# Kernel optimization log

Measured on AMD Instinct MI355X. Metric: run time of the kernel, lower is better.

## Reference

```python
import jax, jax.numpy as jnp
import numpy as np

D, H, WIN, OUT = 3, 64, 8, 32
B, T = 128, 129
IU, JU = np.triu_indices(D, k=1)  # Lyndon pairs i<j at depth 2


def setup_inputs() -> dict:
    key = jax.random.key(0)
    ks = jax.random.split(key, 10)
    ts = jnp.broadcast_to(jnp.linspace(0.0, 1.0, T), (B, T))
    # path-like control values: cumulative sum of small increments
    x = jnp.cumsum(0.1 * jax.random.normal(ks[0], (B, T, D)), axis=1)
    def lin(k, o, i):
        return jax.random.normal(k, (o, i), dtype=jnp.float32) * (1.0 / np.sqrt(i))
    return {
        "ts": ts, "x": x,
        "W0": lin(ks[1], 128, D), "b0": jnp.zeros((128,), jnp.float32),
        "W1": lin(ks[2], 128, 128), "b1": jnp.zeros((128,), jnp.float32),
        "W2": lin(ks[3], H, 128), "b2": jnp.zeros((H,), jnp.float32),
        "V0": lin(ks[4], 128, H), "c0": jnp.zeros((128,), jnp.float32),
        "V1": lin(ks[5], 128, 128), "c1": jnp.zeros((128,), jnp.float32),
        "V2": lin(ks[6], D * H, 128), "c2": jnp.zeros((D * H,), jnp.float32),
        "R": lin(ks[7], OUT, H), "rb": jnp.zeros((OUT,), jnp.float32),
    }


def reference(ts, x, W0, b0, W1, b1, W2, b2, V0, c0, V1, c1, V2, c2, R, rb):
    sp = jax.nn.softplus

    def init_mlp(v):  # R^D -> R^H, Euclidean retract = identity
        return W2 @ sp(W1 @ sp(W0 @ v + b0) + b1) + b2

    def vf_flat(y):  # R^H -> R^{D*H}, final tanh (split_multi_vector_field)
        return jnp.tanh(V2 @ sp(V1 @ sp(V0 @ y + c0) + c1) + c2)

    def F(y):
        # level-1 fields f_i(y) as rows of m: (D, H)
        m = vf_flat(y).reshape(D, H)
        # J[a, b] = D f_b(y) . f_a(y)  via JVPs in directions f_a
        J = jax.vmap(lambda v: jax.jvp(vf_flat, (y,), (v,))[1].reshape(D, H))(m)
        # Lyndon level-2 brackets [f_i, f_j] = Df_j.f_i - Df_i.f_j
        br = J[IU, JU] - J[JU, IU]  # (D*(D-1)/2, H)
        return jnp.concatenate([m, br], axis=0).T  # (H, logsig_size)

    def logsigs_fn(xs):  # depth-2 log-signatures over disjoint windows
        nw = (T - 1) // WIN
        idx = (np.arange(nw) * WIN)[:, None] + np.arange(WIN + 1)[None, :]
        win = xs[idx]
        lvl1 = win[:, -1] - win[:, 0]       # increments
        rel = win[:, :-1] - win[:, :1]      # path relative to window start
        dv = win[:, 1:] - win[:, :-1]       # increments within window
        a = jnp.einsum('nki,nkj->nij', rel, dv)
        area = 0.5 * (a - jnp.swapaxes(a, 1, 2))  # Levy areas
        return jnp.concatenate([lvl1, area[:, IU, JU]], axis=1)

    def solve_one(t, xs):
        h0 = init_mlp(xs[0])
        ls = logsigs_fn(xs)                       # (nw, L)
        t_sig = t[::WIN]                          # window knot times
        slopes = ls / (t_sig[1:] - t_sig[:-1])[:, None]  # dz/dt per window
        slope_steps = jnp.repeat(slopes, WIN, axis=0)    # (T-1, L)
        dts = t[1:] - t[:-1]

        def step(y, inp):  # Heun integration of dy = F(y) dz/dt dt
            dt, s = inp
            k1 = F(y) @ s
            k2 = F(y + dt * k1) @ s
            yn = y + 0.5 * dt * (k1 + k2)
            return yn, yn

        _, ys = jax.lax.scan(step, h0, (dts, slope_steps))
        hidden = jnp.concatenate([h0[None], ys], axis=0)  # (T, H)
        return jnp.tanh(hidden @ R.T + rb)                # evolving readout

    return jax.vmap(solve_one)(ts, x)  # (B, T, OUT)
```

## Files before the change

kernel.cpp:

```cpp
#include <hip/hip_runtime.h>
#include <math.h>

#define BB 128
#define TT 129
#define NSTEP 128
#define NW 16
#define WINW 8
#define OUTD 32

typedef _Float16 h2_t __attribute__((ext_vector_type(2)));

__device__ __forceinline__ float fast_rcp(float v){ return __builtin_amdgcn_rcpf(v); }
__device__ __forceinline__ float softplus_f(float v){ return fmaxf(v,0.f)+__logf(1.f+__expf(-fabsf(v))); }
__device__ __forceinline__ float sigmoid_f(float v){ return fast_rcp(1.f+__expf(-v)); }
__device__ __forceinline__ float tanh_f(float v){
    float ax=fminf(fabsf(v),15.f); float e=__expf(2.f*ax);
    float r=1.f-2.f*fast_rcp(e+1.f); return copysignf(r,v);
}
__device__ __forceinline__ float pack2(float a,float b){
    h2_t h; h.x=(_Float16)a; h.y=(_Float16)b; return __builtin_bit_cast(float,h);
}
__device__ __forceinline__ float dot2c(float wc,float ac,float acc){
    return __builtin_amdgcn_fdot2(__builtin_bit_cast(h2_t,wc),__builtin_bit_cast(h2_t,ac),acc,false);
}
__device__ __forceinline__ float dot2q(float4 wq,float4 aq,float acc){
    acc=dot2c(wq.x,aq.x,acc); acc=dot2c(wq.y,aq.y,acc);
    acc=dot2c(wq.z,aq.z,acc); acc=dot2c(wq.w,aq.w,acc); return acc;
}
#define DOT4(acc,Wv,Av) acc += (Wv).x*(Av).x + (Wv).y*(Av).y + (Wv).z*(Av).z + (Wv).w*(Av).w
#define PIN4(q) asm volatile("" : "+v"((q).x), "+v"((q).y), "+v"((q).z), "+v"((q).w))

#define DPPF(x,ctrl) __builtin_bit_cast(float, __builtin_amdgcn_update_dpp(0, __builtin_bit_cast(int,(x)), (ctrl), 0xF, 0xF, true))
__device__ __forceinline__ float dpp_xor1(float x){ return DPPF(x,0xB1); }
__device__ __forceinline__ float dpp_xor2(float x){ return DPPF(x,0x4E); }
__device__ __forceinline__ float dpp_hmir(float x){ return DPPF(x,0x141); }

__global__ __launch_bounds__(256, 1)
void ncde_solve(const float* __restrict__ ts, const float* __restrict__ x,
                const float* __restrict__ W0, const float* __restrict__ b0,
                const float* __restrict__ W1, const float* __restrict__ b1,
                const float* __restrict__ W2, const float* __restrict__ b2,
                const float* __restrict__ V0, const float* __restrict__ c0,
                const float* __restrict__ V1, const float* __restrict__ c1,
                const float* __restrict__ V2, const float* __restrict__ c2,
                const float* __restrict__ R, const float* __restrict__ rb,
                float* __restrict__ out)
{
    const int b = blockIdx.x;
    const int tid = threadIdx.x;
    const int row2 = tid >> 1, half = tid & 1;
    const int row4 = 128 + (tid >> 2), quad = tid & 3;
    const int prow = tid >> 3, poct = tid & 7;

    __shared__ __align__(16) float RSh[OUTD*68];
    __shared__ __align__(16) float ySh[64], k1Sh[64];
    __shared__ __align__(16) float yp[32], y2p[32];
    __shared__ __align__(16) float a0p[64], a1p[64];
    __shared__ __align__(16) float mp[96];
    __shared__ __align__(16) float u0p[3][64], u1p[3][64];
    __shared__ float mSh[192];
    __shared__ float JfSh[3][192];
    __shared__ float slopesSh[NW][6];
    __shared__ float dtsSh[NSTEP];

    float4 v0p4[4];
    float4 v1p4[8];
    float4 v2p4[8];
    float4 v2q4[4];
    {
        const float4* p0 = (const float4*)(V0 + row2*64 + half*32);
        #pragma unroll
        for (int k=0;k<4;k++){
            float4 a=p0[2*k], c=p0[2*k+1];
            float4 r; r.x=pack2(a.x,a.y); r.y=pack2(a.z,a.w); r.z=pack2(c.x,c.y); r.w=pack2(c.z,c.w);
            v0p4[k]=r;
        }
        const float4* p1 = (const float4*)(V1 + row2*128 + half*64);
        #pragma unroll
        for (int k=0;k<8;k++){
            float4 a=p1[2*k], c=p1[2*k+1];
            float4 r; r.x=pack2(a.x,a.y); r.y=pack2(a.z,a.w); r.z=pack2(c.x,c.y); r.w=pack2(c.z,c.w);
            v1p4[k]=r;
        }
        const float4* p2 = (const float4*)(V2 + row2*128 + half*64);
        #pragma unroll
        for (int k=0;k<8;k++){
            float4 a=p2[2*k], c=p2[2*k+1];
            float4 r; r.x=pack2(a.x,a.y); r.y=pack2(a.z,a.w); r.z=pack2(c.x,c.y); r.w=pack2(c.z,c.w);
            v2p4[k]=r;
        }
        #pragma unroll
        for (int j=0;j<4;j++){
            int g=(quad+j)&3;
            const float4* pg = (const float4*)(V2 + row4*128 + quad*32 + g*8);
            float4 a=pg[0], c=pg[1];
            float4 r; r.x=pack2(a.x,a.y); r.y=pack2(a.z,a.w); r.z=pack2(c.x,c.y); r.w=pack2(c.z,c.w);
            v2q4[j]=r;
        }
        #pragma unroll
        for (int k=0;k<4;k++) PIN4(v0p4[k]);
        #pragma unroll
        for (int k=0;k<8;k++) PIN4(v1p4[k]);
        #pragma unroll
        for (int k=0;k<8;k++) PIN4(v2p4[k]);
        #pragma unroll
        for (int k=0;k<4;k++) PIN4(v2q4[k]);
    }
    const float c0r = c0[row2], c1r = c1[row2], c2a = c2[row2], c2b = c2[row4];
    const float rbp = rb[prow];

    for (int i=tid; i<OUTD*64; i+=256) RSh[(i>>6)*68 + (i&63)] = R[i];
    const float* tsb = ts + b*TT;
    for (int i=tid; i<NSTEP; i+=256) dtsSh[i] = tsb[i+1] - tsb[i];

    if (tid < NW) {
        const int w = tid;
        const float* xs = x + (size_t)(b*TT + w*WINW)*3;
        float x0c[3] = {xs[0], xs[1], xs[2]};
        float prev[3] = {x0c[0], x0c[1], x0c[2]};
        float am01=0.f, am02=0.f, am12=0.f, am10=0.f, am20=0.f, am21=0.f;
        #pragma unroll
        for (int k=0;k<WINW;k++) {
            float cur[3] = {xs[(k+1)*3+0], xs[(k+1)*3+1], xs[(k+1)*3+2]};
            float rel[3], dv[3];
            #pragma unroll
            for (int c=0;c<3;c++){ rel[c]=prev[c]-x0c[c]; dv[c]=cur[c]-prev[c]; }
            am01 += rel[0]*dv[1]; am10 += rel[1]*dv[0];
            am02 += rel[0]*dv[2]; am20 += rel[2]*dv[0];
            am12 += rel[1]*dv[2]; am21 += rel[2]*dv[1];
            prev[0]=cur[0]; prev[1]=cur[1]; prev[2]=cur[2];
        }
        const float invden = 1.f/(tsb[(w+1)*WINW] - tsb[w*WINW]);
        slopesSh[w][0] = (prev[0]-x0c[0])*invden;
        slopesSh[w][1] = (prev[1]-x0c[1])*invden;
        slopesSh[w][2] = (prev[2]-x0c[2])*invden;
        slopesSh[w][3] = 0.5f*(am01-am10)*invden;
        slopesSh[w][4] = 0.5f*(am02-am20)*invden;
        slopesSh[w][5] = 0.5f*(am12-am21)*invden;
    }

    if (tid < 128) {
        const float xv0 = x[(size_t)b*TT*3+0];
        const float xv1 = x[(size_t)b*TT*3+1];
        const float xv2 = x[(size_t)b*TT*3+2];
        float acc = b0[tid] + W0[tid*3]*xv0 + W0[tid*3+1]*xv1 + W0[tid*3+2]*xv2;
        mSh[tid] = softplus_f(acc);
    }
    __syncthreads();
    if (tid < 128) {
        float acc = b1[tid];
        const float4* r = (const float4*)(W1 + tid*128);
        #pragma unroll 8
        for (int k=0;k<32;k++){ float4 wv=r[k]; float4 av=*(const float4*)&mSh[4*k]; DOT4(acc,wv,av); }
        JfSh[0][tid] = softplus_f(acc);
    }
    __syncthreads();
    if (tid < 64) {
        float acc = b2[tid];
        const float4* r = (const float4*)(W2 + tid*128);
        #pragma unroll 8
        for (int k=0;k<32;k++){ float4 wv=r[k]; float4 av=*(const float4*)&JfSh[0][4*k]; DOT4(acc,wv,av); }
        ySh[tid] = acc;
        float p = dpp_xor1(acc);
        if (!(tid & 1)) yp[tid>>1] = pack2(acc, p);
    }
    __syncthreads();

    float sig0r=0.f, sig1r=0.f, dtanAr=0.f, dtanBr=0.f;

    const int tlo = (tid < 128) ? 1 : 0;

    auto Feval = [&](const float* ypIn, bool first, float dt, int w) {
        {
            float zA=0.f, zB=0.f;
            const float4* yb = (const float4*)ypIn + half*4;
            zA=dot2q(v0p4[0],yb[0],zA); zB=dot2q(v0p4[1],yb[1],zB);
            zA=dot2q(v0p4[2],yb[2],zA); zB=dot2q(v0p4[3],yb[3],zB);
            float z = zA + zB;
            z += dpp_xor1(z);
            z += c0r;
            float a = softplus_f(z);
            sig0r = sigmoid_f(z);
            if (!half) ((_Float16*)a0p)[row2] = (_Float16)a;
        }
        __syncthreads();
        {
            float zA=0.f, zB=0.f;
            const float4* ab = (const float4*)a0p + half*8;
            #pragma unroll
            for (int k=0;k<4;k++){ zA=dot2q(v1p4[k],ab[k],zA); }
            #pragma unroll
            for (int k=4;k<8;k++){ zB=dot2q(v1p4[k],ab[k],zB); }
            float z = zA + zB;
            z += dpp_xor1(z);
            z += c1r;
            float a = softplus_f(z);
            sig1r = sigmoid_f(z);
            if (!half) ((_Float16*)a1p)[row2] = (_Float16)a;
        }
        __syncthreads();
        {
            float zA=0.f, zB=0.f;
            const float4* ab = (const float4*)a1p + half*8;
            #pragma unroll
            for (int k=0;k<4;k++){ zA=dot2q(v2p4[k],ab[k],zA); }
            #pragma unroll
            for (int k=4;k<8;k++){ zB=dot2q(v2p4[k],ab[k],zB); }
            float z = zA + zB;
            z += dpp_xor1(z);
            z += c2a;
            float mm = tanh_f(z);
            dtanAr = 1.f - mm*mm;
            if (!half){ mSh[row2]=mm; ((_Float16*)mp)[row2]=(_Float16)mm; }

            float zq = 0.f;
            const float4* a4 = (const float4*)a1p;
            #pragma unroll
            for (int j=0;j<4;j++){ zq=dot2q(v2q4[j], a4[quad*4 + ((quad+j)&3)], zq); }
            zq += dpp_xor1(zq);
            zq += dpp_xor2(zq);
            zq += c2b;
            float mq = tanh_f(zq);
            dtanBr = 1.f - mq*mq;
            if (!quad){ mSh[row4]=mq; ((_Float16*)mp)[row4]=(_Float16)mq; }
        }
        __syncthreads();
        {
            float t0=0.f,t1=0.f,t2=0.f;
            const float4* m0 = (const float4*)mp + half*4;
            const float4* m1 = (const float4*)mp + 8  + half*4;
            const float4* m2 = (const float4*)mp + 16 + half*4;
            #pragma unroll
            for (int k=0;k<4;k++){ t0=dot2q(v0p4[k],m0[k],t0); t1=dot2q(v0p4[k],m1[k],t1); t2=dot2q(v0p4[k],m2[k],t2); }
            t0 += dpp_xor1(t0);
            t1 += dpp_xor1(t1);
            t2 += dpp_xor1(t2);
            if (!half){
                ((_Float16*)&u0p[0][0])[row2]=(_Float16)(sig0r*t0);
                ((_Float16*)&u0p[1][0])[row2]=(_Float16)(sig0r*t1);
                ((_Float16*)&u0p[2][0])[row2]=(_Float16)(sig0r*t2);
            }
        }
        __syncthreads();
        {
            float t0=0.f,t1=0.f,t2=0.f;
            const float4* q0 = (const float4*)&u0p[0][0] + half*8;
            const float4* q1 = (const float4*)&u0p[1][0] + half*8;
            const float4* q2 = (const float4*)&u0p[2][0] + half*8;
            #pragma unroll
            for (int k=0;k<8;k++){ t0=dot2q(v1p4[k],q0[k],t0); t1=dot2q(v1p4[k],q1[k],t1); t2=dot2q(v1p4[k],q2[k],t2); }
            t0 += dpp_xor1(t0);
            t1 += dpp_xor1(t1);
            t2 += dpp_xor1(t2);
            if (!half){
                ((_Float16*)&u1p[0][0])[row2]=(_Float16)(sig1r*t0);
                ((_Float16*)&u1p[1][0])[row2]=(_Float16)(sig1r*t1);
                ((_Float16*)&u1p[2][0])[row2]=(_Float16)(sig1r*t2);
            }
        }
        __syncthreads();
        {
            float tl=0.f, t2v=0.f;
            const float4* ql = (const float4*)&u1p[tlo][0] + half*8;
            const float4* q2 = (const float4*)&u1p[2][0]   + half*8;
            #pragma unroll
            for (int k=0;k<8;k++){ tl=dot2q(v2p4[k],ql[k],tl); t2v=dot2q(v2p4[k],q2[k],t2v); }
            tl  += dpp_xor1(tl);
            t2v += dpp_xor1(t2v);
            if (!half){ JfSh[tlo][row2]=dtanAr*tl; JfSh[2][row2]=dtanAr*t2v; }

            float s0=0.f,s1=0.f;
            const float4* w0 = (const float4*)&u1p[0][0];
            const float4* w1 = (const float4*)&u1p[1][0];
            #pragma unroll
            for (int j=0;j<4;j++){
                const int idx = quad*4 + ((quad+j)&3);
                s0=dot2q(v2q4[j],w0[idx],s0); s1=dot2q(v2q4[j],w1[idx],s1);
            }
            s0 += dpp_xor1(s0); s0 += dpp_xor2(s0);
            s1 += dpp_xor1(s1); s1 += dpp_xor2(s1);
            if (!quad){ JfSh[0][row4]=dtanBr*s0; JfSh[1][row4]=dtanBr*s1; }
        }
        __syncthreads();
        if (tid < 64) {
            const int h = tid;
            const float s0=slopesSh[w][0], s1=slopesSh[w][1], s2=slopesSh[w][2],
                        s3=slopesSh[w][3], s4=slopesSh[w][4], s5=slopesSh[w][5];
            float kk = mSh[h]*s0 + mSh[64+h]*s1 + mSh[128+h]*s2;
            kk += s3*(JfSh[0][64+h]  - JfSh[1][h]);
            kk += s4*(JfSh[0][128+h] - JfSh[2][h]);
            kk += s5*(JfSh[1][128+h] - JfSh[2][64+h]);
            if (first){
                k1Sh[h] = kk;
                float y2 = ySh[h] + dt*kk;
                float p = dpp_xor1(y2);
                if (!(h&1)) y2p[h>>1] = pack2(y2, p);
            } else {
                float yn = ySh[h] + 0.5f*dt*(k1Sh[h] + kk);
                ySh[h] = yn;
                float p = dpp_xor1(yn);
                if (!(h&1)) yp[h>>1] = pack2(yn, p);
            }
        }
        __syncthreads();
    };

    auto proj = [&](int stp) {
        const float4* rr = (const float4*)(RSh + prow*68 + poct*8);
        const float4* yy = (const float4*)(ySh + poct*8);
        float pacc = 0.f;
        DOT4(pacc, rr[0], yy[0]); DOT4(pacc, rr[1], yy[1]);
        pacc += dpp_xor1(pacc);
        pacc += dpp_xor2(pacc);
        pacc += dpp_hmir(pacc);
        if (!poct) out[(size_t)(b*TT + stp)*OUTD + prow] = tanh_f(pacc + rbp);
    };

    for (int step=0; step<NSTEP; ++step) {
        proj(step);
        const float dt = dtsSh[step];
        const int w = step >> 3;
        Feval(yp,  true,  dt, w);
        Feval(y2p, false, dt, w);
    }
    proj(NSTEP);
}

extern "C" void kernel_launch(void* const* d_in, const int* in_sizes, int n_in,
                              void* d_out, int out_size, void* d_ws, size_t ws_size,
                              hipStream_t stream) {
    const float* ts = (const float*)d_in[0];
    const float* x  = (const float*)d_in[1];
    const float* W0 = (const float*)d_in[2];
    const float* b0 = (const float*)d_in[3];
    const float* W1 = (const float*)d_in[4];
    const float* b1 = (const float*)d_in[5];
    const float* W2 = (const float*)d_in[6];
    const float* b2 = (const float*)d_in[7];
    const float* V0 = (const float*)d_in[8];
    const float* c0 = (const float*)d_in[9];
    const float* V1 = (const float*)d_in[10];
    const float* c1 = (const float*)d_in[11];
    const float* V2 = (const float*)d_in[12];
    const float* c2 = (const float*)d_in[13];
    const float* R  = (const float*)d_in[14];
    const float* rb = (const float*)d_in[15];
    float* out = (float*)d_out;

    ncde_solve<<<dim3(BB), dim3(256), 0, stream>>>(
        ts, x, W0, b0, W1, b1, W2, b2, V0, c0, V1, c1, V2, c2, R, rb, out);
}
```

Before: 687.1 us.

## Remap work so each thread quad owns rows across all layers, fusing bracket combine

Reorganises the per-step MLP and JVP work so each group of four threads owns hidden row r together with its 64- and 128-offset partners in every layer. Weights are held in registers in this new row-blocked layout, and reductions use two DPP stages. As a result the Lie-bracket combine and Heun update run in registers in the last stage, with y and k1 kept per thread, instead of going through a separate JfSh/mSh stage and barrier. This removes one __syncthreads per F evaluation and some shared-memory traffic. In exchange it uses more registers per thread and adds extra DPP reduction steps.

After: 617.2 us. -10.2%, faster.

```diff
diff --git a/kernel.cpp b/kernel.cpp
--- a/kernel.cpp
+++ b/kernel.cpp
@@ -28,7 +28,7 @@
     acc=dot2c(wq.z,aq.z,acc); acc=dot2c(wq.w,aq.w,acc); return acc;
 }
 #define DOT4(acc,Wv,Av) acc += (Wv).x*(Av).x + (Wv).y*(Av).y + (Wv).z*(Av).z + (Wv).w*(Av).w
-#define PIN4(q) asm volatile("" : "+v"((q).x), "+v"((q).y), "+v"((q).z), "+v"((q).w))
+#define PIN4(v) asm volatile("" : "+v"((v).x), "+v"((v).y), "+v"((v).z), "+v"((v).w))
 
 #define DPPF(x,ctrl) __builtin_bit_cast(float, __builtin_amdgcn_update_dpp(0, __builtin_bit_cast(int,(x)), (ctrl), 0xF, 0xF, true))
 __device__ __forceinline__ float dpp_xor1(float x){ return DPPF(x,0xB1); }
@@ -48,65 +48,59 @@
 {
     const int b = blockIdx.x;
     const int tid = threadIdx.x;
-    const int row2 = tid >> 1, half = tid & 1;
-    const int row4 = 128 + (tid >> 2), quad = tid & 3;
+    const int r = tid >> 2, q = tid & 3;
     const int prow = tid >> 3, poct = tid & 7;
 
     __shared__ __align__(16) float RSh[OUTD*68];
-    __shared__ __align__(16) float ySh[64], k1Sh[64];
+    __shared__ __align__(16) float ySh[64];
     __shared__ __align__(16) float yp[32], y2p[32];
-    __shared__ __align__(16) float a0p[64], a1p[64];
-    __shared__ __align__(16) float mp[96];
-    __shared__ __align__(16) float u0p[3][64], u1p[3][64];
-    __shared__ float mSh[192];
-    __shared__ float JfSh[3][192];
+    __shared__ __align__(16) float a0H[64], a1H[64];
+    __shared__ __align__(16) float mpH[96];
+    __shared__ __align__(16) float u0H[192], u1H[192];
     __shared__ float slopesSh[NW][6];
     __shared__ float dtsSh[NSTEP];
 
-    float4 v0p4[4];
-    float4 v1p4[8];
-    float4 v2p4[8];
-    float4 v2q4[4];
+    float4 v0c[2][2], v1c[2][4], v2c[3][4];
     {
-        const float4* p0 = (const float4*)(V0 + row2*64 + half*32);
-        #pragma unroll
-        for (int k=0;k<4;k++){
-            float4 a=p0[2*k], c=p0[2*k+1];
-            float4 r; r.x=pack2(a.x,a.y); r.y=pack2(a.z,a.w); r.z=pack2(c.x,c.y); r.w=pack2(c.z,c.w);
-            v0p4[k]=r;
-        }
-        const float4* p1 = (const float4*)(V1 + row2*128 + half*64);
-        #pragma unroll
-        for (int k=0;k<8;k++){
-            float4 a=p1[2*k], c=p1[2*k+1];
-            float4 r; r.x=pack2(a.x,a.y); r.y=pack2(a.z,a.w); r.z=pack2(c.x,c.y); r.w=pack2(c.z,c.w);
-            v1p4[k]=r;
-        }
-        const float4* p2 = (const float4*)(V2 + row2*128 + half*64);
-        #pragma unroll
-        for (int k=0;k<8;k++){
-            float4 a=p2[2*k], c=p2[2*k+1];
-            float4 r; r.x=pack2(a.x,a.y); r.y=pack2(a.z,a.w); r.z=pack2(c.x,c.y); r.w=pack2(c.z,c.w);
-            v2p4[k]=r;
-        }
-        #pragma unroll
-        for (int j=0;j<4;j++){
-            int g=(quad+j)&3;
-            const float4* pg = (const float4*)(V2 + row4*128 + quad*32 + g*8);
-            float4 a=pg[0], c=pg[1];
-            float4 r; r.x=pack2(a.x,a.y); r.y=pack2(a.z,a.w); r.z=pack2(c.x,c.y); r.w=pack2(c.z,c.w);
-            v2q4[j]=r;
-        }
-        #pragma unroll
-        for (int k=0;k<4;k++) PIN4(v0p4[k]);
-        #pragma unroll
-        for (int k=0;k<8;k++) PIN4(v1p4[k]);
-        #pragma unroll
-        for (int k=0;k<8;k++) PIN4(v2p4[k]);
-        #pragma unroll
-        for (int k=0;k<4;k++) PIN4(v2q4[k]);
-    }
-    const float c0r = c0[row2], c1r = c1[row2], c2a = c2[row2], c2b = c2[row4];
+        auto pkld = [](const float* src)->float4{
+            const float4* p=(const float4*)src;
+            float4 a=p[0], c=p[1];
+            float4 rr; rr.x=pack2(a.x,a.y); rr.y=pack2(a.z,a.w); rr.z=pack2(c.x,c.y); rr.w=pack2(c.z,c.w);
+            return rr;
+        };
+        #pragma unroll
+        for (int i=0;i<2;i++){
+            const float* base = V0 + (r+64*i)*64 + q*16;
+            v0c[i][0]=pkld(base); v0c[i][1]=pkld(base+8);
+        }
+        #pragma unroll
+        for (int i=0;i<2;i++){
+            const float* base = V1 + (r+64*i)*128 + q*32;
+            #pragma unroll
+            for (int k=0;k<4;k++) v1c[i][k]=pkld(base+8*k);
+        }
+        #pragma unroll
+        for (int i=0;i<3;i++){
+            const float* base = V2 + (r+64*i)*128 + q*32;
+            #pragma unroll
+            for (int k=0;k<4;k++) v2c[i][k]=pkld(base+8*k);
+        }
+        #pragma unroll
+        for (int i=0;i<2;i++){ PIN4(v0c[i][0]); PIN4(v0c[i][1]); }
+        #pragma unroll
+        for (int i=0;i<2;i++){
+            #pragma unroll
+            for (int k=0;k<4;k++) PIN4(v1c[i][k]);
+        }
+        #pragma unroll
+        for (int i=0;i<3;i++){
+            #pragma unroll
+            for (int k=0;k<4;k++) PIN4(v2c[i][k]);
+        }
+    }
+    const float c0A=c0[r], c0B=c0[64+r];
+    const float c1A=c1[r], c1B=c1[64+r];
+    const float c2A=c2[r], c2B=c2[64+r], c2C=c2[128+r];
     const float rbp = rb[prow];
 
     for (int i=tid; i<OUTD*64; i+=256) RSh[(i>>6)*68 + (i&63)] = R[i];
@@ -144,162 +138,167 @@
         const float xv1 = x[(size_t)b*TT*3+1];
         const float xv2 = x[(size_t)b*TT*3+2];
         float acc = b0[tid] + W0[tid*3]*xv0 + W0[tid*3+1]*xv1 + W0[tid*3+2]*xv2;
-        mSh[tid] = softplus_f(acc);
+        u0H[tid] = softplus_f(acc);
     }
     __syncthreads();
     if (tid < 128) {
         float acc = b1[tid];
-        const float4* r = (const float4*)(W1 + tid*128);
+        const float4* rw = (const float4*)(W1 + tid*128);
         #pragma unroll 8
-        for (int k=0;k<32;k++){ float4 wv=r[k]; float4 av=*(const float4*)&mSh[4*k]; DOT4(acc,wv,av); }
-        JfSh[0][tid] = softplus_f(acc);
+        for (int k=0;k<32;k++){ float4 wv=rw[k]; float4 av=*(const float4*)&u0H[4*k]; DOT4(acc,wv,av); }
+        u1H[tid] = softplus_f(acc);
     }
     __syncthreads();
     if (tid < 64) {
         float acc = b2[tid];
-        const float4* r = (const float4*)(W2 + tid*128);
+        const float4* rw = (const float4*)(W2 + tid*128);
         #pragma unroll 8
-        for (int k=0;k<32;k++){ float4 wv=r[k]; float4 av=*(const float4*)&JfSh[0][4*k]; DOT4(acc,wv,av); }
+        for (int k=0;k<32;k++){ float4 wv=rw[k]; float4 av=*(const float4*)&u1H[4*k]; DOT4(acc,wv,av); }
         ySh[tid] = acc;
-        float p = dpp_xor1(acc);
-        if (!(tid & 1)) yp[tid>>1] = pack2(acc, p);
+        ((_Float16*)yp)[tid] = (_Float16)acc;
     }
     __syncthreads();
 
-    float sig0r=0.f, sig1r=0.f, dtanAr=0.f, dtanBr=0.f;
-
-    const int tlo = (tid < 128) ? 1 : 0;
-
-    auto Feval = [&](const float* ypIn, bool first, float dt, int w) {
-        {
+    float yreg = ySh[r];
+    float k1r = 0.f;
+    float S0,S1,S2,S3,S4,S5;
+
+    auto Feval = [&](const float* ypIn, bool first, float dtc) {
+        float sig0A,sig0B,sig1A,sig1B,mA,mB,mC,dtA,dtB,dtC;
+        {
+            const float4* Y = (const float4*)ypIn + q*2;
+            float4 y0=Y[0], y1=Y[1];
             float zA=0.f, zB=0.f;
-            const float4* yb = (const float4*)ypIn + half*4;
-            zA=dot2q(v0p4[0],yb[0],zA); zB=dot2q(v0p4[1],yb[1],zB);
-            zA=dot2q(v0p4[2],yb[2],zA); zB=dot2q(v0p4[3],yb[3],zB);
-            float z = zA + zB;
-            z += dpp_xor1(z);
-            z += c0r;
-            float a = softplus_f(z);
-            sig0r = sigmoid_f(z);
-            if (!half) ((_Float16*)a0p)[row2] = (_Float16)a;
-        }
-        __syncthreads();
-        {
+            zA=dot2q(v0c[0][0],y0,zA); zA=dot2q(v0c[0][1],y1,zA);
+            zB=dot2q(v0c[1][0],y0,zB); zB=dot2q(v0c[1][1],y1,zB);
+            zA += dpp_xor1(zA); zA += dpp_xor2(zA); zA += c0A;
+            zB += dpp_xor1(zB); zB += dpp_xor2(zB); zB += c0B;
+            sig0A=sigmoid_f(zA); sig0B=sigmoid_f(zB);
+            if (!q){
+                ((_Float16*)a0H)[r]    = (_Float16)softplus_f(zA);
+                ((_Float16*)a0H)[64+r] = (_Float16)softplus_f(zB);
+            }
+        }
+        __syncthreads();
+        {
+            const float4* A = (const float4*)a0H + q*4;
+            float4 a0=A[0],a1=A[1],a2=A[2],a3=A[3];
             float zA=0.f, zB=0.f;
-            const float4* ab = (const float4*)a0p + half*8;
-            #pragma unroll
-            for (int k=0;k<4;k++){ zA=dot2q(v1p4[k],ab[k],zA); }
-            #pragma unroll
-            for (int k=4;k<8;k++){ zB=dot2q(v1p4[k],ab[k],zB); }
-            float z = zA + zB;
-            z += dpp_xor1(z);
-            z += c1r;
-            float a = softplus_f(z);
-            sig1r = sigmoid_f(z);
-            if (!half) ((_Float16*)a1p)[row2] = (_Float16)a;
-        }
-        __syncthreads();
-        {
-            float zA=0.f, zB=0.f;
-            const float4* ab = (const float4*)a1p + half*8;
-            #pragma unroll
-            for (int k=0;k<4;k++){ zA=dot2q(v2p4[k],ab[k],zA); }
-            #pragma unroll
-            for (int k=4;k<8;k++){ zB=dot2q(v2p4[k],ab[k],zB); }
-            float z = zA + zB;
-            z += dpp_xor1(z);
-            z += c2a;
-            float mm = tanh_f(z);
-            dtanAr = 1.f - mm*mm;
-            if (!half){ mSh[row2]=mm; ((_Float16*)mp)[row2]=(_Float16)mm; }
-
-            float zq = 0.f;
-            const float4* a4 = (const float4*)a1p;
-            #pragma unroll
-            for (int j=0;j<4;j++){ zq=dot2q(v2q4[j], a4[quad*4 + ((quad+j)&3)], zq); }
-            zq += dpp_xor1(zq);
-            zq += dpp_xor2(zq);
-            zq += c2b;
-            float mq = tanh_f(zq);
-            dtanBr = 1.f - mq*mq;
-            if (!quad){ mSh[row4]=mq; ((_Float16*)mp)[row4]=(_Float16)mq; }
-        }
-        __syncthreads();
-        {
-            float t0=0.f,t1=0.f,t2=0.f;
-            const float4* m0 = (const float4*)mp + half*4;
-            const float4* m1 = (const float4*)mp + 8  + half*4;
-            const float4* m2 = (const float4*)mp + 16 + half*4;
-            #pragma unroll
-            for (int k=0;k<4;k++){ t0=dot2q(v0p4[k],m0[k],t0); t1=dot2q(v0p4[k],m1[k],t1); t2=dot2q(v0p4[k],m2[k],t2); }
-            t0 += dpp_xor1(t0);
-            t1 += dpp_xor1(t1);
-            t2 += dpp_xor1(t2);
-            if (!half){
-                ((_Float16*)&u0p[0][0])[row2]=(_Float16)(sig0r*t0);
-                ((_Float16*)&u0p[1][0])[row2]=(_Float16)(sig0r*t1);
-                ((_Float16*)&u0p[2][0])[row2]=(_Float16)(sig0r*t2);
-            }
-        }
-        __syncthreads();
-        {
-            float t0=0.f,t1=0.f,t2=0.f;
-            const float4* q0 = (const float4*)&u0p[0][0] + half*8;
-            const float4* q1 = (const float4*)&u0p[1][0] + half*8;
-            const float4* q2 = (const float4*)&u0p[2][0] + half*8;
-            #pragma unroll
-            for (int k=0;k<8;k++){ t0=dot2q(v1p4[k],q0[k],t0); t1=dot2q(v1p4[k],q1[k],t1); t2=dot2q(v1p4[k],q2[k],t2); }
-            t0 += dpp_xor1(t0);
-            t1 += dpp_xor1(t1);
-            t2 += dpp_xor1(t2);
-            if (!half){
-                ((_Float16*)&u1p[0][0])[row2]=(_Float16)(sig1r*t0);
-                ((_Float16*)&u1p[1][0])[row2]=(_Float16)(sig1r*t1);
-                ((_Float16*)&u1p[2][0])[row2]=(_Float16)(sig1r*t2);
-            }
-        }
-        __syncthreads();
-        {
-            float tl=0.f, t2v=0.f;
-            const float4* ql = (const float4*)&u1p[tlo][0] + half*8;
-            const float4* q2 = (const float4*)&u1p[2][0]   + half*8;
-            #pragma unroll
-            for (int k=0;k<8;k++){ tl=dot2q(v2p4[k],ql[k],tl); t2v=dot2q(v2p4[k],q2[k],t2v); }
-            tl  += dpp_xor1(tl);
-            t2v += dpp_xor1(t2v);
-            if (!half){ JfSh[tlo][row2]=dtanAr*tl; JfSh[2][row2]=dtanAr*t2v; }
-
-            float s0=0.f,s1=0.f;
-            const float4* w0 = (const float4*)&u1p[0][0];
-            const float4* w1 = (const float4*)&u1p[1][0];
-            #pragma unroll
-            for (int j=0;j<4;j++){
-                const int idx = quad*4 + ((quad+j)&3);
-                s0=dot2q(v2q4[j],w0[idx],s0); s1=dot2q(v2q4[j],w1[idx],s1);
-            }
-            s0 += dpp_xor1(s0); s0 += dpp_xor2(s0);
-            s1 += dpp_xor1(s1); s1 += dpp_xor2(s1);
-            if (!quad){ JfSh[0][row4]=dtanBr*s0; JfSh[1][row4]=dtanBr*s1; }
-        }
-        __syncthreads();
-        if (tid < 64) {
-            const int h = tid;
-            const float s0=slopesSh[w][0], s1=slopesSh[w][1], s2=slopesSh[w][2],
-                        s3=slopesSh[w][3], s4=slopesSh[w][4], s5=slopesSh[w][5];
-            float kk = mSh[h]*s0 + mSh[64+h]*s1 + mSh[128+h]*s2;
-            kk += s3*(JfSh[0][64+h]  - JfSh[1][h]);
-            kk += s4*(JfSh[0][128+h] - JfSh[2][h]);
-            kk += s5*(JfSh[1][128+h] - JfSh[2][64+h]);
+            zA=dot2q(v1c[0][0],a0,zA); zA=dot2q(v1c[0][1],a1,zA); zA=dot2q(v1c[0][2],a2,zA); zA=dot2q(v1c[0][3],a3,zA);
+            zB=dot2q(v1c[1][0],a0,zB); zB=dot2q(v1c[1][1],a1,zB); zB=dot2q(v1c[1][2],a2,zB); zB=dot2q(v1c[1][3],a3,zB);
+            zA += dpp_xor1(zA); zA += dpp_xor2(zA); zA += c1A;
+            zB += dpp_xor1(zB); zB += dpp_xor2(zB); zB += c1B;
+            sig1A=sigmoid_f(zA); sig1B=sigmoid_f(zB);
+            if (!q){
+                ((_Float16*)a1H)[r]    = (_Float16)softplus_f(zA);
+                ((_Float16*)a1H)[64+r] = (_Float16)softplus_f(zB);
+            }
+        }
+        __syncthreads();
+        {
+            const float4* A = (const float4*)a1H + q*4;
+            float4 a0=A[0],a1=A[1],a2=A[2],a3=A[3];
+            float zA=0.f, zB=0.f, zC=0.f;
+            zA=dot2q(v2c[0][0],a0,zA); zA=dot2q(v2c[0][1],a1,zA); zA=dot2q(v2c[0][2],a2,zA); zA=dot2q(v2c[0][3],a3,zA);
+            zB=dot2q(v2c[1][0],a0,zB); zB=dot2q(v2c[1][1],a1,zB); zB=dot2q(v2c[1][2],a2,zB); zB=dot2q(v2c[1][3],a3,zB);
+            zC=dot2q(v2c[2][0],a0,zC); zC=dot2q(v2c[2][1],a1,zC); zC=dot2q(v2c[2][2],a2,zC); zC=dot2q(v2c[2][3],a3,zC);
+            zA += dpp_xor1(zA); zA += dpp_xor2(zA);
+            zB += dpp_xor1(zB); zB += dpp_xor2(zB);
+            zC += dpp_xor1(zC); zC += dpp_xor2(zC);
+            mA=tanh_f(zA+c2A); mB=tanh_f(zB+c2B); mC=tanh_f(zC+c2C);
+            dtA=1.f-mA*mA; dtB=1.f-mB*mB; dtC=1.f-mC*mC;
+            if (!q){
+                ((_Float16*)mpH)[r]     = (_Float16)mA;
+                ((_Float16*)mpH)[64+r]  = (_Float16)mB;
+                ((_Float16*)mpH)[128+r] = (_Float16)mC;
+            }
+        }
+        __syncthreads();
+        {
+            const float4* M = (const float4*)mpH;
+            float4 g00=M[q*2], g01=M[q*2+1];
+            float4 g10=M[8+q*2], g11=M[8+q*2+1];
+            float4 g20=M[16+q*2], g21=M[16+q*2+1];
+            float t0A=0.f,t1A=0.f,t2A=0.f,t0B=0.f,t1B=0.f,t2B=0.f;
+            t0A=dot2q(v0c[0][0],g00,t0A); t0A=dot2q(v0c[0][1],g01,t0A);
+            t1A=dot2q(v0c[0][0],g10,t1A); t1A=dot2q(v0c[0][1],g11,t1A);
+            t2A=dot2q(v0c[0][0],g20,t2A); t2A=dot2q(v0c[0][1],g21,t2A);
+            t0B=dot2q(v0c[1][0],g00,t0B); t0B=dot2q(v0c[1][1],g01,t0B);
+            t1B=dot2q(v0c[1][0],g10,t1B); t1B=dot2q(v0c[1][1],g11,t1B);
+            t2B=dot2q(v0c[1][0],g20,t2B); t2B=dot2q(v0c[1][1],g21,t2B);
+            t0A += dpp_xor1(t0A); t0A += dpp_xor2(t0A);
+            t1A += dpp_xor1(t1A); t1A += dpp_xor2(t1A);
+            t2A += dpp_xor1(t2A); t2A += dpp_xor2(t2A);
+            t0B += dpp_xor1(t0B); t0B += dpp_xor2(t0B);
+            t1B += dpp_xor1(t1B); t1B += dpp_xor2(t1B);
+            t2B += dpp_xor1(t2B); t2B += dpp_xor2(t2B);
+            if (!q){
+                ((_Float16*)u0H)[r]      = (_Float16)(sig0A*t0A);
+                ((_Float16*)u0H)[64+r]   = (_Float16)(sig0B*t0B);
+                ((_Float16*)u0H)[128+r]  = (_Float16)(sig0A*t1A);
+                ((_Float16*)u0H)[192+r]  = (_Float16)(sig0B*t1B);
+                ((_Float16*)u0H)[256+r]  = (_Float16)(sig0A*t2A);
+                ((_Float16*)u0H)[320+r]  = (_Float16)(sig0B*t2B);
+            }
+        }
+        __syncthreads();
+        {
+            const float4* U = (const float4*)u0H;
+            float4 g0[4],g1[4],g2[4];
+            #pragma unroll
+            for (int k=0;k<4;k++){ g0[k]=U[q*4+k]; g1[k]=U[16+q*4+k]; g2[k]=U[32+q*4+k]; }
+            float t0A=0.f,t1A=0.f,t2A=0.f,t0B=0.f,t1B=0.f,t2B=0.f;
+            #pragma unroll
+            for (int k=0;k<4;k++){
+                float4 wa=v1c[0][k], wb=v1c[1][k];
+                t0A=dot2q(wa,g0[k],t0A); t1A=dot2q(wa,g1[k],t1A); t2A=dot2q(wa,g2[k],t2A);
+                t0B=dot2q(wb,g0[k],t0B); t1B=dot2q(wb,g1[k],t1B); t2B=dot2q(wb,g2[k],t2B);
+            }
+            t0A += dpp_xor1(t0A); t0A += dpp_xor2(t0A);
+            t1A += dpp_xor1(t1A); t1A += dpp_xor2(t1A);
+            t2A += dpp_xor1(t2A); t2A += dpp_xor2(t2A);
+            t0B += dpp_xor1(t0B); t0B += dpp_xor2(t0B);
+            t1B += dpp_xor1(t1B); t1B += dpp_xor2(t1B);
+            t2B += dpp_xor1(t2B); t2B += dpp_xor2(t2B);
+            if (!q){
+                ((_Float16*)u1H)[r]      = (_Float16)(sig1A*t0A);
+                ((_Float16*)u1H)[64+r]   = (_Float16)(sig1B*t0B);
+                ((_Float16*)u1H)[128+r]  = (_Float16)(sig1A*t1A);
+                ((_Float16*)u1H)[192+r]  = (_Float16)(sig1B*t1B);
+                ((_Float16*)u1H)[256+r]  = (_Float16)(sig1A*t2A);
+                ((_Float16*)u1H)[320+r]  = (_Float16)(sig1B*t2B);
+            }
+        }
+        __syncthreads();
+        {
+            const float4* U = (const float4*)u1H;
+            float4 g0[4],g1[4],g2[4];
+            #pragma unroll
+            for (int k=0;k<4;k++){ g0[k]=U[q*4+k]; g1[k]=U[16+q*4+k]; g2[k]=U[32+q*4+k]; }
+            float J1r=0.f,J2r=0.f,J0m=0.f,J2m=0.f,J0t=0.f,J1t=0.f;
+            #pragma unroll
+            for (int k=0;k<4;k++){
+                float4 wa=v2c[0][k], wb=v2c[1][k], wc=v2c[2][k];
+                J1r=dot2q(wa,g1[k],J1r); J2r=dot2q(wa,g2[k],J2r);
+                J0m=dot2q(wb,g0[k],J0m); J2m=dot2q(wb,g2[k],J2m);
+                J0t=dot2q(wc,g0[k],J0t); J1t=dot2q(wc,g1[k],J1t);
+            }
+            J1r += dpp_xor1(J1r); J1r += dpp_xor2(J1r);
+            J2r += dpp_xor1(J2r); J2r += dpp_xor2(J2r);
+            J0m += dpp_xor1(J0m); J0m += dpp_xor2(J0m);
+            J2m += dpp_xor1(J2m); J2m += dpp_xor2(J2m);
+            J0t += dpp_xor1(J0t); J0t += dpp_xor2(J0t);
+            J1t += dpp_xor1(J1t); J1t += dpp_xor2(J1t);
+            J1r*=dtA; J2r*=dtA; J0m*=dtB; J2m*=dtB; J0t*=dtC; J1t*=dtC;
+            float kk = mA*S0 + mB*S1 + mC*S2
+                     + S3*(J0m - J1r) + S4*(J0t - J2r) + S5*(J1t - J2m);
             if (first){
-                k1Sh[h] = kk;
-                float y2 = ySh[h] + dt*kk;
-                float p = dpp_xor1(y2);
-                if (!(h&1)) y2p[h>>1] = pack2(y2, p);
+                k1r = kk;
+                float y2 = yreg + dtc*kk;
+                if (!q) ((_Float16*)y2p)[r] = (_Float16)y2;
             } else {
-                float yn = ySh[h] + 0.5f*dt*(k1Sh[h] + kk);
-                ySh[h] = yn;
-                float p = dpp_xor1(yn);
-                if (!(h&1)) yp[h>>1] = pack2(yn, p);
+                yreg += 0.5f*dtc*(k1r + kk);
+                if (!q){ ((_Float16*)yp)[r] = (_Float16)yreg; ySh[r] = yreg; }
             }
         }
         __syncthreads();
@@ -318,10 +317,12 @@
 
     for (int step=0; step<NSTEP; ++step) {
         proj(step);
-        const float dt = dtsSh[step];
         const int w = step >> 3;
-        Feval(yp,  true,  dt, w);
-        Feval(y2p, false, dt, w);
+        S0=slopesSh[w][0]; S1=slopesSh[w][1]; S2=slopesSh[w][2];
+        S3=slopesSh[w][3]; S4=slopesSh[w][4]; S5=slopesSh[w][5];
+        const float dtc = dtsSh[step];
+        Feval(yp,  true,  dtc);
+        Feval(y2p, false, dtc);
     }
     proj(NSTEP);
 }
```
